# Kernel tuning notes

Hardware: AMD Instinct MI355X
Metric: run time of the kernel (lower is better)

## Reference

```python
import jax, jax.numpy as jnp
import numpy as np

BLOCK = 64       # _aether_cfg['block_size']
JL_DIM = 32      # epsilon_jl_bridge d_out
EPS_GOV = 0.5    # fixed governor eps (governor.target)
ROPE_BASE = 10000.0
RMS_EPS = 1e-6


def _normalize(x, axis=-1):
    n = jnp.sqrt(jnp.sum(x * x, axis=axis, keepdims=True))
    return x / jnp.maximum(n, 1e-12)


def _rms_norm(x):
    return x * jax.lax.rsqrt(jnp.mean(x * x, axis=-1, keepdims=True) + RMS_EPS)


def _rope(x, cos, sin):
    half = x.shape[-1] // 2
    x1, x2 = x[..., :half], x[..., half:]
    return jnp.concatenate([x1 * cos + x2 * sin, -x1 * sin + x2 * cos], axis=-1)


def setup_inputs() -> dict:
    key = jax.random.key(0)
    ks = jax.random.split(key, 6)
    B, S, Dm, H = 2, 2048, 2048, 16
    sc = 1.0 / np.sqrt(Dm)
    x = jax.random.normal(ks[0], (B, S, Dm), jnp.float32)
    Wq = jax.random.normal(ks[1], (Dm, Dm), jnp.float32) * sc
    Wk = jax.random.normal(ks[2], (Dm, Dm), jnp.float32) * sc
    Wv = jax.random.normal(ks[3], (Dm, Dm), jnp.float32) * sc
    Wo = jax.random.normal(ks[4], (Dm, Dm), jnp.float32) * sc
    q_gain = jnp.ones((H,), jnp.float32)
    return {"x": x, "Wq": Wq, "Wk": Wk, "Wv": Wv, "Wo": Wo, "q_gain": q_gain}


def reference(x, Wq, Wk, Wv, Wo, q_gain):
    B, S, Dm = x.shape
    H = q_gain.shape[0]
    Dh = Dm // H

    # QKV projections (bias-free linear, torch weight layout [out,in])
    q = (x @ Wq.T).reshape(B, S, H, Dh).transpose(0, 2, 1, 3)  # (B,H,S,Dh)
    k = (x @ Wk.T).reshape(B, S, H, Dh).transpose(0, 2, 1, 3)
    v = (x @ Wv.T).reshape(B, S, H, Dh).transpose(0, 2, 1, 3)

    # RoPE tables
    inv_freq = 1.0 / (ROPE_BASE ** (jnp.arange(0, Dh, 2, dtype=jnp.float32) / Dh))
    freqs = jnp.outer(jnp.arange(S, dtype=jnp.float32), inv_freq)  # (S,Dh/2)
    cos = jnp.cos(freqs)[None, None]
    sin = jnp.sin(freqs)[None, None]

    q = _rope(_rms_norm(q), cos, sin) * q_gain[None, :, None, None]
    k = _rope(_rms_norm(k), cos, sin)

    # --- aether sparse SDPA: JL block bounds -> top-k blocks -> gather -> SDPA ---
    N = S // BLOCK  # number of KV blocks (static)
    proj = jax.random.normal(jax.random.key(42), (Dh, JL_DIM), jnp.float32) / np.sqrt(JL_DIM)

    q_proj = _normalize(q.mean(axis=2, keepdims=True) @ proj)          # (B,H,1,JL)
    k_blocks = k.reshape(B, H, N, BLOCK, Dh)
    k_proj = _normalize(k_blocks @ proj)                               # (B,H,N,BLOCK,JL)
    centroids = _normalize(k_proj.mean(axis=3))                        # (B,H,N,JL)
    radii = jnp.clip(
        1.0 - jnp.min(jnp.sum(k_proj * centroids[:, :, :, None, :], axis=-1), axis=-1),
        0.0, 1.0)                                                      # (B,H,N)
    ub = jnp.einsum('bhqj,bhnj->bhqn', q_proj, centroids) + radii[:, :, None, :]
    scores = ub[:, :, 0, :]                                            # (B,H,N)
    # force-include the last two blocks (union in the original code)
    scores = scores.at[:, :, N - 2:].set(jnp.inf)

    n_keep = max(2, int(N * min(1.0, EPS_GOV))) + 2                    # static
    _, top_idx = jax.lax.top_k(scores, n_keep)                         # (B,H,n_keep)
    top_idx = jnp.sort(top_idx, axis=-1)
    idx = (top_idx[..., None] * BLOCK + jnp.arange(BLOCK)).reshape(B, H, -1)  # (B,H,K)

    k_s = jnp.take_along_axis(k, idx[..., None], axis=2)               # (B,H,K,Dh)
    v_s = jnp.take_along_axis(v, idx[..., None], axis=2)

    att = jax.nn.softmax(
        jnp.einsum('bhqd,bhkd->bhqk', q, k_s) / np.sqrt(Dh), axis=-1)  # (B,H,S,K)
    y = jnp.einsum('bhqk,bhkd->bhqd', att, v_s)                        # (B,H,S,Dh)

    y = y.transpose(0, 2, 1, 3).reshape(B, S, Dm)
    return y @ Wo.T
```

## Files before the change

kernel.cpp:

```cpp
#include <hip/hip_runtime.h>
#include <hip/hip_bf16.h>

#define B_ 2
#define S_ 2048
#define DM 2048
#define H_ 16
#define DH 128
#define NBLK 32
#define NKEEP 18
#define BH (B_ * H_)

typedef __attribute__((ext_vector_type(8))) short short8;
typedef __attribute__((ext_vector_type(8))) _Float16 f16x8;
typedef __attribute__((ext_vector_type(4))) _Float16 f16x4;
typedef __attribute__((ext_vector_type(4))) float f32x4;

#define GLOAD16(gp, lp)                                                        \
  __builtin_amdgcn_global_load_lds(                                            \
      (const __attribute__((address_space(1))) unsigned int*)(const void*)(gp),\
      (__attribute__((address_space(3))) unsigned int*)(void*)(lp), 16, 0, 0)

__device__ __forceinline__ unsigned short f32_to_bf16(float f) {
  unsigned u = __float_as_uint(f);
  unsigned r = (u + 0x7fffu + ((u >> 16) & 1u)) >> 16;
  return (unsigned short)r;
}
__device__ __forceinline__ float bf16_to_f32(unsigned short h) {
  return __uint_as_float(((unsigned)h) << 16);
}

__device__ __forceinline__ unsigned rotl32(unsigned x, int r) {
  return (x << r) | (x >> (32 - r));
}

__device__ __forceinline__ float erfinv_f32(float x) {
  float w = -log1pf(-x * x);
  float p;
  if (w < 5.0f) {
    w -= 2.5f;
    p = 2.81022636e-08f;
    p = fmaf(p, w, 3.43273939e-07f);
    p = fmaf(p, w, -3.5233877e-06f);
    p = fmaf(p, w, -4.39150654e-06f);
    p = fmaf(p, w, 0.00021858087f);
    p = fmaf(p, w, -0.00125372503f);
    p = fmaf(p, w, -0.00417768164f);
    p = fmaf(p, w, 0.246640727f);
    p = fmaf(p, w, 1.50140941f);
  } else {
    w = sqrtf(w) - 3.0f;
    p = -0.000200214257f;
    p = fmaf(p, w, 0.000100950558f);
    p = fmaf(p, w, 0.00134934322f);
    p = fmaf(p, w, -0.00367342844f);
    p = fmaf(p, w, 0.00573950773f);
    p = fmaf(p, w, -0.0076224613f);
    p = fmaf(p, w, 0.00943887047f);
    p = fmaf(p, w, 1.00167406f);
    p = fmaf(p, w, 2.83297682f);
  }
  return p * x;
}

__device__ __forceinline__ float bits_to_normal(unsigned b) {
  float f = __uint_as_float((b >> 9) | 0x3f800000u) - 1.0f;
  const float lo = -0.9999999403953552f;
  float u = fmaxf(lo, fmaf(f, 2.0f, lo));
  return 1.4142135623730951f * erfinv_f32(u);
}

__global__ void proj_kernel(float* __restrict__ proj) {
  int i = blockIdx.x * blockDim.x + threadIdx.x;
  if (i >= 4096) return;
  unsigned k0 = 0u, k1 = 42u;
  unsigned k2 = 0x1BD11BDAu ^ k0 ^ k1;
  unsigned x0 = 0u, x1 = (unsigned)i;
  x0 += k0; x1 += k1;
#define QR(r) { x0 += x1; x1 = rotl32(x1, r); x1 ^= x0; }
  QR(13) QR(15) QR(26) QR(6)   x0 += k1; x1 += k2 + 1u;
  QR(17) QR(29) QR(16) QR(24)  x0 += k2; x1 += k0 + 2u;
  QR(13) QR(15) QR(26) QR(6)   x0 += k0; x1 += k1 + 3u;
  QR(17) QR(29) QR(16) QR(24)  x0 += k1; x1 += k2 + 4u;
  QR(13) QR(15) QR(26) QR(6)   x0 += k2; x1 += k0 + 5u;
#undef QR
  proj[i] = bits_to_normal(x0 ^ x1) / 5.656854249492381f;
}

__global__ void rope_table_kernel(float* __restrict__ cosb, float* __restrict__ sinb) {
  int s = blockIdx.x;
  int j = threadIdx.x;
  double e = (double)(2 * j) / 128.0;
  double invf = 1.0 / pow(10000.0, e);
  float freq = (float)s * (float)invf;
  cosb[s * 64 + j] = (float)cos((double)freq);
  sinb[s * 64 + j] = (float)sin((double)freq);
}

__global__ __launch_bounds__(256) void split_x3_kernel(const float* __restrict__ in,
                                                       unsigned short* __restrict__ hi,
                                                       unsigned short* __restrict__ lo,
                                                       _Float16* __restrict__ f16,
                                                       int n4) {
  int i = blockIdx.x * blockDim.x + threadIdx.x;
  if (i >= n4) return;
  float4 v = ((const float4*)in)[i];
  ushort4 hv, lv;
  f16x4 fv;
  hv.x = f32_to_bf16(v.x); lv.x = f32_to_bf16(v.x - bf16_to_f32(hv.x)); fv[0] = (_Float16)v.x;
  hv.y = f32_to_bf16(v.y); lv.y = f32_to_bf16(v.y - bf16_to_f32(hv.y)); fv[1] = (_Float16)v.y;
  hv.z = f32_to_bf16(v.z); lv.z = f32_to_bf16(v.z - bf16_to_f32(hv.z)); fv[2] = (_Float16)v.z;
  hv.w = f32_to_bf16(v.w); lv.w = f32_to_bf16(v.w - bf16_to_f32(hv.w)); fv[3] = (_Float16)v.w;
  ((ushort4*)hi)[i] = hv;
  ((ushort4*)lo)[i] = lv;
  ((f16x4*)f16)[i] = fv;
}

__global__ __launch_bounds__(256) void split_kernel(const float* __restrict__ in,
                                                    unsigned short* __restrict__ hi,
                                                    unsigned short* __restrict__ lo,
                                                    int n4) {
  int i = blockIdx.x * blockDim.x + threadIdx.x;
  if (i >= n4) return;
  float4 v = ((const float4*)in)[i];
  ushort4 hv, lv;
  hv.x = f32_to_bf16(v.x); lv.x = f32_to_bf16(v.x - bf16_to_f32(hv.x));
  hv.y = f32_to_bf16(v.y); lv.y = f32_to_bf16(v.y - bf16_to_f32(hv.y));
  hv.z = f32_to_bf16(v.z); lv.z = f32_to_bf16(v.z - bf16_to_f32(hv.z));
  hv.w = f32_to_bf16(v.w); lv.w = f32_to_bf16(v.w - bf16_to_f32(hv.w));
  ((ushort4*)hi)[i] = hv;
  ((ushort4*)lo)[i] = lv;
}

__global__ __launch_bounds__(256) void split_f16_kernel(const float* __restrict__ in,
                                                        _Float16* __restrict__ f16,
                                                        int n4) {
  int i = blockIdx.x * blockDim.x + threadIdx.x;
  if (i >= n4) return;
  float4 v = ((const float4*)in)[i];
  f16x4 fv;
  fv[0] = (_Float16)v.x; fv[1] = (_Float16)v.y;
  fv[2] = (_Float16)v.z; fv[3] = (_Float16)v.w;
  ((f16x4*)f16)[i] = fv;
}

__global__ __launch_bounds__(512, 2) void mfma_gemm_k_sk(const unsigned short* __restrict__ Ahi,
                                                         const unsigned short* __restrict__ Alo,
                                                         const unsigned short* __restrict__ Whi,
                                                         const unsigned short* __restrict__ Wlo,
                                                         float* __restrict__ kp0,
                                                         float* __restrict__ kp1) {
  __shared__ char smem[131072];
  const int t = threadIdx.x, l = t & 63, w = t >> 6;
  const int lin = blockIdx.z * 128 + blockIdx.y * 8 + blockIdx.x;
  const int swz = (lin & 7) * 32 + (lin >> 3);
  const int kz = swz >> 7;
  const int idx = swz & 127;
  const int n0 = (idx & 7) * 256;
  const int m0 = (idx >> 3) * 256;
  const int kbase = kz * 1024;
  float* C = kz ? kp1 : kp0;
  const int wm = w >> 2, wn = w & 3;
  const int lr = l & 15;
  const int lg8 = (l >> 4) * 8;
  const size_t rstep = (size_t)16 * DM;

  const unsigned short* gAh = Ahi + (size_t)(m0 + w * 32 + lr) * DM + lg8;
  const unsigned short* gAl = Alo + (size_t)(m0 + w * 32 + lr) * DM + lg8;
  const unsigned short* gBh = Whi + (size_t)(n0 + w * 32 + lr) * DM + lg8;
  const unsigned short* gBl = Wlo + (size_t)(n0 + w * 32 + lr) * DM + lg8;

  auto STAGE = [&](int k0, int c) {
    char* base = smem + c * 65536 + w * 2048;
    GLOAD16(gAh + k0, base);
    GLOAD16(gAh + rstep + k0, base + 1024);
    GLOAD16(gAl + k0, base + 16384);
    GLOAD16(gAl + rstep + k0, base + 16384 + 1024);
    GLOAD16(gBh + k0, base + 32768);
    GLOAD16(gBh + rstep + k0, base + 32768 + 1024);
    GLOAD16(gBl + k0, base + 49152);
    GLOAD16(gBl + rstep + k0, base + 49152 + 1024);
  };

  f32x4 acc[8][4];
#pragma unroll
  for (int i = 0; i < 8; ++i)
#pragma unroll
    for (int j = 0; j < 4; ++j) acc[i][j] = (f32x4){0.f, 0.f, 0.f, 0.f};

  STAGE(kbase, 0);
  int cur = 0;

  for (int k0 = kbase; k0 < kbase + 1024; k0 += 32) {
    if (k0 + 32 < kbase + 1024) {
      STAGE(k0 + 32, cur ^ 1);
      asm volatile("s_waitcnt vmcnt(8)" ::: "memory");
    } else {
      asm volatile("s_waitcnt vmcnt(0)" ::: "memory");
    }
    __builtin_amdgcn_s_barrier();

    char* buf = smem + cur * 65536;
    short8 bh[4], bl[4];
#pragma unroll
    for (int f = 0; f < 4; ++f) {
      bh[f] = *(const short8*)(buf + 32768 + (wn * 4 + f) * 1024 + l * 16);
      bl[f] = *(const short8*)(buf + 49152 + (wn * 4 + f) * 1024 + l * 16);
    }
    __builtin_amdgcn_s_setprio(1);
#pragma unroll
    for (int mp = 0; mp < 4; ++mp) {
      short8 ah0 = *(const short8*)(buf + (wm * 8 + 2 * mp) * 1024 + l * 16);
      short8 ah1 = *(const short8*)(buf + (wm * 8 + 2 * mp + 1) * 1024 + l * 16);
      short8 al0 = *(const short8*)(buf + 16384 + (wm * 8 + 2 * mp) * 1024 + l * 16);
      short8 al1 = *(const short8*)(buf + 16384 + (wm * 8 + 2 * mp + 1) * 1024 + l * 16);
#pragma unroll
      for (int n = 0; n < 4; ++n) {
        acc[2 * mp][n] = __builtin_amdgcn_mfma_f32_16x16x32_bf16(ah0, bh[n], acc[2 * mp][n], 0, 0, 0);
        acc[2 * mp][n] = __builtin_amdgcn_mfma_f32_16x16x32_bf16(ah0, bl[n], acc[2 * mp][n], 0, 0, 0);
        acc[2 * mp][n] = __builtin_amdgcn_mfma_f32_16x16x32_bf16(al0, bh[n], acc[2 * mp][n], 0, 0, 0);
      }
#pragma unroll
      for (int n = 0; n < 4; ++n) {
        acc[2 * mp + 1][n] = __builtin_amdgcn_mfma_f32_16x16x32_bf16(ah1, bh[n], acc[2 * mp + 1][n], 0, 0, 0);
        acc[2 * mp + 1][n] = __builtin_amdgcn_mfma_f32_16x16x32_bf16(ah1, bl[n], acc[2 * mp + 1][n], 0, 0, 0);
        acc[2 * mp + 1][n] = __builtin_amdgcn_mfma_f32_16x16x32_bf16(al1, bh[n], acc[2 * mp + 1][n], 0, 0, 0);
      }
    }
    __builtin_amdgcn_s_setprio(0);
    __builtin_amdgcn_s_barrier();
    cur ^= 1;
  }

#pragma unroll
  for (int m = 0; m < 8; ++m) {
    int row0 = m0 + wm * 128 + m * 16 + (l >> 4) * 4;
#pragma unroll
    for (int n = 0; n < 4; ++n) {
      int col = n0 + wn * 64 + n * 16 + (l & 15);
      int h = col >> 7, d = col & 127;
#pragma unroll
      for (int r = 0; r < 4; ++r) {
        int mm = row0 + r;
        int b = mm >> 11, s = mm & (S_ - 1);
        C[(((size_t)(b * H_ + h) * S_) + s) * DH + d] = acc[m][n][r];
      }
    }
  }
}

__global__ __launch_bounds__(512, 2) void mfma_gemm_qv(const _Float16* __restrict__ A,
                                                       const _Float16* __restrict__ W,
                                                       float* __restrict__ Cq,
                                                       _Float16* __restrict__ vt) {
  __shared__ char smem[65536];
  const int t = threadIdx.x, l = t & 63, w = t >> 6;
  const int lin = blockIdx.y * gridDim.x + blockIdx.x;
  const int swz = (lin & 7) * 32 + (lin >> 3);
  const int n0 = (swz & 15) * 256;
  const int m0 = (swz >> 4) * 256;
  const int wm = w >> 2, wn = w & 3;
  const int lr = l & 15;
  const int lg8 = (l >> 4) * 8;
  const size_t rstep = (size_t)16 * DM;

  const _Float16* gA = A + (size_t)(m0 + w * 32 + lr) * DM + lg8;
  const _Float16* gB = W + (size_t)(n0 + w * 32 + lr) * DM + lg8;

  auto STAGE = [&](int k0, int c) {
    char* base = smem + c * 32768 + w * 2048;
    GLOAD16(gA + k0, base);
    GLOAD16(gA + rstep + k0, base + 1024);
    GLOAD16(gB + k0, base + 16384);
    GLOAD16(gB + rstep + k0, base + 16384 + 1024);
  };

  f32x4 acc[8][4];
#pragma unroll
  for (int i = 0; i < 8; ++i)
#pragma unroll
    for (int j = 0; j < 4; ++j) acc[i][j] = (f32x4){0.f, 0.f, 0.f, 0.f};

  STAGE(0, 0);
  int cur = 0;

  for (int k0 = 0; k0 < DM; k0 += 32) {
    if (k0 + 32 < DM) {
      STAGE(k0 + 32, cur ^ 1);
      asm volatile("s_waitcnt vmcnt(4)" ::: "memory");
    } else {
      asm volatile("s_waitcnt vmcnt(0)" ::: "memory");
    }
    __builtin_amdgcn_s_barrier();

    char* buf = smem + cur * 32768;
    f16x8 b[4];
#pragma unroll
    for (int j = 0; j < 4; ++j)
      b[j] = *(const f16x8*)(buf + 16384 + (wn * 4 + j) * 1024 + l * 16);
    __builtin_amdgcn_s_setprio(1);
#pragma unroll
    for (int i = 0; i < 8; ++i) {
      f16x8 a = *(const f16x8*)(buf + (wm * 8 + i) * 1024 + l * 16);
#pragma unroll
      for (int j = 0; j < 4; ++j)
        acc[i][j] = __builtin_amdgcn_mfma_f32_16x16x32_f16(a, b[j], acc[i][j], 0, 0, 0);
    }
    __builtin_amdgcn_s_setprio(0);
    __builtin_amdgcn_s_barrier();
    cur ^= 1;
  }

#pragma unroll
  for (int m = 0; m < 8; ++m) {
    int row0 = m0 + wm * 128 + m * 16 + (l >> 4) * 4;
#pragma unroll
    for (int n = 0; n < 4; ++n) {
      int col = n0 + wn * 64 + n * 16 + (l & 15);
      if (col < DM) {
        int h = col >> 7, d = col & 127;
#pragma unroll
        for (int r = 0; r < 4; ++r) {
          int mm = row0 + r;
          int b2 = mm >> 11, s = mm & (S_ - 1);
          Cq[(((size_t)(b2 * H_ + h) * S_) + s) * DH + d] = acc[m][n][r];
        }
      } else {
        int vcol = col - DM;
        int h = vcol >> 7, d = vcol & 127;
        int b2 = row0 >> 11, s0 = row0 & (S_ - 1);
        f16x4 vv;
        vv[0] = (_Float16)acc[m][n][0];
        vv[1] = (_Float16)acc[m][n][1];
        vv[2] = (_Float16)acc[m][n][2];
        vv[3] = (_Float16)acc[m][n][3];
        *(f16x4*)(vt + (((size_t)(b2 * H_ + h)) * DH + d) * S_ + s0) = vv;
      }
    }
  }
}

template <int MODE>
__global__ __launch_bounds__(256) void mfma_gemm_f16(const _Float16* __restrict__ A,
                                                     const _Float16* __restrict__ W,
                                                     void* __restrict__ Cout) {
  __shared__ char smem[65536];
  const int t = threadIdx.x, l = t & 63, w = t >> 6;
  const int lin = blockIdx.y * gridDim.x + blockIdx.x;
  const int cpx = (gridDim.x * gridDim.y) >> 3;
  const int swz = (lin & 7) * cpx + (lin >> 3);
  const int n0 = (swz % gridDim.x) * 128;
  const int m0 = (swz / gridDim.x) * 128;
  const int wm = w >> 1, wn = w & 1;
  const int lr = l & 15;
  const int lg8 = (l >> 4) * 8;

  auto STAGE = [&](int k0, int c) {
    char* base = smem + c * 32768;
#pragma unroll
    for (int f0 = 0; f0 < 4; ++f0) {
      int f = w * 4 + f0;
      int rb = f >> 1, kh = f & 1;
      GLOAD16(A + (size_t)(m0 + rb * 16 + lr) * DM + k0 + kh * 32 + lg8,
              base + f * 1024);
      GLOAD16(W + (size_t)(n0 + rb * 16 + lr) * DM + k0 + kh * 32 + lg8,
              base + 16384 + f * 1024);
    }
  };

  f32x4 acc[4][4];
#pragma unroll
  for (int i = 0; i < 4; ++i)
#pragma unroll
    for (int j = 0; j < 4; ++j) acc[i][j] = (f32x4){0.f, 0.f, 0.f, 0.f};

  STAGE(0, 0);
  int cur = 0;

  for (int k0 = 0; k0 < DM; k0 += 64) {
    if (k0 + 64 < DM) {
      STAGE(k0 + 64, cur ^ 1);
      asm volatile("s_waitcnt vmcnt(8)" ::: "memory");
    } else {
      asm volatile("s_waitcnt vmcnt(0)" ::: "memory");
    }
    __builtin_amdgcn_s_barrier();

    char* buf = smem + cur * 32768;
    f16x8 a[4][2], b[4][2];
#pragma unroll
    for (int i = 0; i < 4; ++i)
#pragma unroll
      for (int kh = 0; kh < 2; ++kh) {
        a[i][kh] = *(const f16x8*)(buf + ((wm * 4 + i) * 2 + kh) * 1024 + l * 16);
        b[i][kh] = *(const f16x8*)(buf + 16384 + ((wn * 4 + i) * 2 + kh) * 1024 + l * 16);
      }
    __builtin_amdgcn_s_setprio(1);
#pragma unroll
    for (int i = 0; i < 4; ++i)
#pragma unroll
      for (int j = 0; j < 4; ++j) {
        acc[i][j] = __builtin_amdgcn_mfma_f32_16x16x32_f16(a[i][0], b[j][0], acc[i][j], 0, 0, 0);
        acc[i][j] = __builtin_amdgcn_mfma_f32_16x16x32_f16(a[i][1], b[j][1], acc[i][j], 0, 0, 0);
      }
    __builtin_amdgcn_s_setprio(0);
    __builtin_amdgcn_s_barrier();
    cur ^= 1;
  }

#pragma unroll
  for (int i = 0; i < 4; ++i) {
    int row0 = m0 + wm * 64 + i * 16 + (l >> 4) * 4;
#pragma unroll
    for (int j = 0; j < 4; ++j) {
      int col = n0 + wn * 64 + j * 16 + (l & 15);
      if constexpr (MODE == 1) {
        float* C = (float*)Cout;
#pragma unroll
        for (int r = 0; r < 4; ++r)
          C[(size_t)(row0 + r) * DM + col] = acc[i][j][r];
      }
    }
  }
}

__global__ __launch_bounds__(256) void rmsrope_k_kernel(float* __restrict__ k,
                                                        const float* __restrict__ kp1,
                                                        _Float16* __restrict__ kf,
                                                        const float* __restrict__ cosb,
                                                        const float* __restrict__ sinb) {
  int w = threadIdx.x >> 6;
  int lane = threadIdx.x & 63;
  long r = (long)blockIdx.x * 4 + w;
  float* p = k + r * DH;
  const float* p1 = kp1 + r * DH;
  int s = (int)(r & (S_ - 1));
  float x1 = p[lane] + p1[lane];
  float x2 = p[lane + 64] + p1[lane + 64];
  float ss = fmaf(x1, x1, x2 * x2);
#pragma unroll
  for (int off = 32; off; off >>= 1) ss += __shfl_xor(ss, off);
  float rms = rsqrtf(ss * (1.0f / 128.0f) + 1e-6f);
  float n1 = x1 * rms, n2 = x2 * rms;
  float c = cosb[s * 64 + lane], sn = sinb[s * 64 + lane];
  float o1 = fmaf(n1, c, n2 * sn);
  float o2 = fmaf(-n1, sn, n2 * c);
  p[lane] = o1;
  p[lane + 64] = o2;
  kf[r * DH + lane] = (_Float16)o1;
  kf[r * DH + lane + 64] = (_Float16)o2;
}

__global__ __launch_bounds__(256) void rmsrope_q_kernel(float* __restrict__ q,
                                                        const float* __restrict__ cosb,
                                                        const float* __restrict__ sinb,
                                                        const float* __restrict__ qg) {
  int w = threadIdx.x >> 6;
  int lane = threadIdx.x & 63;
  long r = (long)blockIdx.x * 4 + w;
  float* p = q + r * DH;
  int s = (int)(r & (S_ - 1));
  int h = (int)((r >> 11) & (H_ - 1));
  float x1 = p[lane], x2 = p[lane + 64];
  float ss = fmaf(x1, x1, x2 * x2);
#pragma unroll
  for (int off = 32; off; off >>= 1) ss += __shfl_xor(ss, off);
  float rms = rsqrtf(ss * (1.0f / 128.0f) + 1e-6f);
  float n1 = x1 * rms, n2 = x2 * rms;
  float c = cosb[s * 64 + lane], sn = sinb[s * 64 + lane];
  float g = qg[h];
  float o1 = fmaf(n1, c, n2 * sn) * g;
  float o2 = fmaf(-n1, sn, n2 * c) * g;
  p[lane] = o1;
  p[lane + 64] = o2;
}

__global__ __launch_bounds__(256) void qmean_part_kernel(const float* __restrict__ q,
                                                         float* __restrict__ partial) {
  __shared__ float red[256];
  const int bh = blockIdx.x >> 4, chunk = blockIdx.x & 15;
  const int t = threadIdx.x;
  const int d = t & 127, half = t >> 7;
  const float* qb = q + ((size_t)bh * S_ + chunk * 128 + half * 64) * DH;
  float sum = 0.0f;
#pragma unroll 4
  for (int s = 0; s < 64; ++s) sum += qb[(size_t)s * DH + d];
  red[t] = sum;
  __syncthreads();
  if (t < 128) partial[(size_t)blockIdx.x * 128 + t] = red[t] + red[t + 128];
}

__global__ void qproj_kernel(const float* __restrict__ partial,
                             const float* __restrict__ proj,
                             float* __restrict__ qp) {
  __shared__ float meanq[128];
  __shared__ float qps[32];
  __shared__ float nrm;
  const int bh = blockIdx.x, t = threadIdx.x;
  float s = 0.0f;
#pragma unroll
  for (int c = 0; c < 16; ++c) s += partial[((size_t)bh * 16 + c) * 128 + t];
  meanq[t] = s * (1.0f / 2048.0f);
  __syncthreads();
  if (t < 32) {
    float sum = 0.0f;
    for (int d = 0; d < 128; ++d) sum = fmaf(meanq[d], proj[d * 32 + t], sum);
    qps[t] = sum;
  }
  __syncthreads();
  if (t == 0) {
    float sum = 0.0f;
    for (int j = 0; j < 32; ++j) sum += qps[j] * qps[j];
    nrm = 1.0f / fmaxf(sqrtf(sum), 1e-12f);
  }
  __syncthreads();
  if (t < 32) qp[bh * 32 + t] = qps[t] * nrm;
}

__global__ __launch_bounds__(256) void kscore_kernel(const float* __restrict__ k,
                                                     const float* __restrict__ proj,
                                                     const float* __restrict__ qp,
                                                     float* __restrict__ scores) {
  __shared__ float ps[128][32];
  __shared__ float kp[64][33];
  __shared__ float cent[33];
  __shared__ float nrm;
  const int bh = blockIdx.x >> 5, n = blockIdx.x & 31;
  const int t = threadIdx.x;
  for (int i = t; i < 4096; i += 256) ps[i >> 5][i & 31] = proj[i];
  const float* kn = k + ((size_t)bh * S_ + n * 64) * DH;
  __syncthreads();
  {
    int row = t >> 2, j0 = (t & 3) * 8;
    float accv[8];
#pragma unroll
    for (int jj = 0; jj < 8; ++jj) accv[jj] = 0.0f;
#pragma unroll 4
    for (int d = 0; d < 128; ++d) {
      float kv = kn[(size_t)row * DH + d];
#pragma unroll
      for (int jj = 0; jj < 8; ++jj) accv[jj] = fmaf(kv, ps[d][j0 + jj], accv[jj]);
    }
#pragma unroll
    for (int jj = 0; jj < 8; ++jj) kp[row][j0 + jj] = accv[jj];
  }
  __syncthreads();
  if (t < 64) {
    float sum = 0.0f;
    for (int j = 0; j < 32; ++j) sum += kp[t][j] * kp[t][j];
    float scl = 1.0f / fmaxf(sqrtf(sum), 1e-12f);
    for (int j = 0; j < 32; ++j) kp[t][j] *= scl;
  }
  __syncthreads();
  if (t < 32) {
    float sum = 0.0f;
    for (int r2 = 0; r2 < 64; ++r2) sum += kp[r2][t];
    cent[t] = sum * (1.0f / 64.0f);
  }
  __syncthreads();
  if (t == 0) {
    float sum = 0.0f;
    for (int j = 0; j < 32; ++j) sum += cent[j] * cent[j];
    nrm = 1.0f / fmaxf(sqrtf(sum), 1e-12f);
  }
  __syncthreads();
  if (t < 32) cent[t] *= nrm;
  __syncthreads();
  if (t < 64) {
    float dt = 0.0f;
    for (int j = 0; j < 32; ++j) dt = fmaf(kp[t][j], cent[j], dt);
#pragma unroll
    for (int off = 32; off; off >>= 1) dt = fminf(dt, __shfl_xor(dt, off));
    if (t == 0) {
      float radius = fminf(fmaxf(1.0f - dt, 0.0f), 1.0f);
      float dq = 0.0f;
      for (int j = 0; j < 32; ++j) dq = fmaf(qp[bh * 32 + j], cent[j], dq);
      scores[bh * 32 + n] = dq + radius;
    }
  }
}

__global__ void topk_kernel(const float* __restrict__ scores, int* __restrict__ top_idx) {
  if (threadIdx.x != 0) return;
  const int bh = blockIdx.x;
  float sc[NBLK];
  for (int j = 0; j < NBLK; ++j) sc[j] = scores[bh * 32 + j];
  sc[NBLK - 2] = INFINITY;
  sc[NBLK - 1] = INFINITY;
  int chosen[NKEEP];
  bool used[NBLK];
  for (int j = 0; j < NBLK; ++j) used[j] = false;
  for (int kk = 0; kk < NKEEP; ++kk) {
    int best = -1;
    float bv = 0.0f;
    for (int j = 0; j < NBLK; ++j)
      if (!used[j] && (best < 0 || sc[j] > bv)) { bv = sc[j]; best = j; }
    used[best] = true;
    chosen[kk] = best;
  }
  for (int a = 1; a < NKEEP; ++a) {
    int v2 = chosen[a], b2 = a - 1;
    while (b2 >= 0 && chosen[b2] > v2) { chosen[b2 + 1] = chosen[b2]; --b2; }
    chosen[b2 + 1] = v2;
  }
  for (int a = 0; a < NKEEP; ++a) top_idx[bh * NKEEP + a] = chosen[a];
}

__global__ __launch_bounds__(256) void attn_mfma_kernel(const float* __restrict__ q,
                                                        const _Float16* __restrict__ kf,
                                                        const _Float16* __restrict__ vt,
                                                        const int* __restrict__ top_idx,
                                                        _Float16* __restrict__ yf) {
  __shared__ char lds[74752];
  const int bh = blockIdx.x >> 5;
  const int qt = blockIdx.x & 31;
  const int t = threadIdx.x, l = t & 63, w = t >> 6;
  const int lr = l & 15, lg = l >> 4;
  const float scale = 0.08838834764831843f;

  f16x8 qf[4];
  {
    const float* qbase = q + ((size_t)(bh * S_ + qt * 64 + w * 16 + lr)) * DH + lg * 8;
#pragma unroll
    for (int dc = 0; dc < 4; ++dc) {
      float4 v0 = *(const float4*)(qbase + dc * 32);
      float4 v1 = *(const float4*)(qbase + dc * 32 + 4);
      f16x8 h;
      h[0] = (_Float16)v0.x; h[1] = (_Float16)v0.y; h[2] = (_Float16)v0.z; h[3] = (_Float16)v0.w;
      h[4] = (_Float16)v1.x; h[5] = (_Float16)v1.y; h[6] = (_Float16)v1.z; h[7] = (_Float16)v1.w;
      qf[dc] = h;
    }
  }

  float m_[4] = {-INFINITY, -INFINITY, -INFINITY, -INFINITY};
  float ls[4] = {0.f, 0.f, 0.f, 0.f};
  f32x4 yacc[8];
#pragma unroll
  for (int dt = 0; dt < 8; ++dt) yacc[dt] = (f32x4){0.f, 0.f, 0.f, 0.f};

  char* Pw = lds + 65536 + w * 2304;

  const _Float16* kb0 = kf + (size_t)bh * S_ * DH;
  const _Float16* vb0 = vt + (size_t)bh * DH * S_;
  const int* idxp = top_idx + bh * NKEEP;

  auto STAGE = [&](int blk, int c) {
    char* base = lds + c * 32768;
#pragma unroll
    for (int f0 = 0; f0 < 4; ++f0) {
      int f = w * 4 + f0;
      int kt = f >> 2, dc = f & 3;
      GLOAD16(kb0 + (size_t)(blk * 64 + kt * 16 + lr) * DH + dc * 32 + lg * 8,
              base + f * 1024);
      int K0 = f >> 3, dt = f & 7;
      GLOAD16(vb0 + (size_t)(dt * 16 + lr) * S_ + blk * 64 + K0 * 32 + lg * 8,
              base + 16384 + f * 1024);
    }
  };

  int cur = 0;
  STAGE(idxp[0], 0);

  for (int it = 0; it < NKEEP; ++it) {
    if (it + 1 < NKEEP) {
      STAGE(idxp[it + 1], cur ^ 1);
      asm volatile("s_waitcnt vmcnt(8)" ::: "memory");
    } else {
      asm volatile("s_waitcnt vmcnt(0)" ::: "memory");
    }
    __builtin_amdgcn_s_barrier();
    char* buf = lds + cur * 32768;

    f32x4 sacc[4];
#pragma unroll
    for (int kt = 0; kt < 4; ++kt) sacc[kt] = (f32x4){0.f, 0.f, 0.f, 0.f};
    __builtin_amdgcn_s_setprio(1);
#pragma unroll
    for (int kt = 0; kt < 4; ++kt)
#pragma unroll
      for (int dc = 0; dc < 4; ++dc) {
        f16x8 kfr = *(const f16x8*)(buf + (kt * 4 + dc) * 1024 + l * 16);
        sacc[kt] = __builtin_amdgcn_mfma_f32_16x16x32_f16(qf[dc], kfr, sacc[kt], 0, 0, 0);
      }
    __builtin_amdgcn_s_setprio(0);

    float p[4][4];
#pragma unroll
    for (int r = 0; r < 4; ++r) {
      float mt = fmaxf(fmaxf(sacc[0][r], sacc[1][r]), fmaxf(sacc[2][r], sacc[3][r])) * scale;
#pragma unroll
      for (int off = 1; off < 16; off <<= 1) mt = fmaxf(mt, __shfl_xor(mt, off));
      float mn = fmaxf(m_[r], mt);
      float corr = __expf(m_[r] - mn);
      float rs = 0.f;
#pragma unroll
      for (int kt = 0; kt < 4; ++kt) {
        p[kt][r] = __expf(fmaf(sacc[kt][r], scale, -mn));
        rs += p[kt][r];
      }
#pragma unroll
      for (int off = 1; off < 16; off <<= 1) rs += __shfl_xor(rs, off);
      ls[r] = ls[r] * corr + rs;
      m_[r] = mn;
#pragma unroll
      for (int dt = 0; dt < 8; ++dt) yacc[dt][r] *= corr;
    }

#pragma unroll
    for (int kt = 0; kt < 4; ++kt)
#pragma unroll
      for (int r = 0; r < 4; ++r)
        *(_Float16*)(Pw + (lg * 4 + r) * 144 + (kt * 16 + lr) * 2) = (_Float16)p[kt][r];

    __builtin_amdgcn_s_setprio(1);
#pragma unroll
    for (int K0 = 0; K0 < 2; ++K0) {
      f16x8 pa = *(const f16x8*)(Pw + lr * 144 + K0 * 64 + lg * 16);
#pragma unroll
      for (int dt = 0; dt < 8; ++dt) {
        f16x8 vf = *(const f16x8*)(buf + 16384 + (K0 * 8 + dt) * 1024 + l * 16);
        yacc[dt] = __builtin_amdgcn_mfma_f32_16x16x32_f16(pa, vf, yacc[dt], 0, 0, 0);
      }
    }
    __builtin_amdgcn_s_setprio(0);

    __builtin_amdgcn_s_barrier();
    cur ^= 1;
  }

  const int b = bh >> 4, h = bh & (H_ - 1);
  float inv[4];
#pragma unroll
  for (int r = 0; r < 4; ++r) inv[r] = 1.0f / ls[r];
#pragma unroll
  for (int r = 0; r < 4; ++r) {
    int srow = qt * 64 + w * 16 + lg * 4 + r;
    size_t off0 = ((size_t)b * S_ + srow) * DM + h * DH + lr;
#pragma unroll
    for (int dt = 0; dt < 8; ++dt)
      yf[off0 + dt * 16] = (_Float16)(yacc[dt][r] * inv[r]);
  }
}

extern "C" void kernel_launch(void* const* d_in, const int* in_sizes, int n_in,
                              void* d_out, int out_size, void* d_ws, size_t ws_size,
                              hipStream_t stream) {
  const float* x  = (const float*)d_in[0];
  const float* Wq = (const float*)d_in[1];
  const float* Wk = (const float*)d_in[2];
  const float* Wv = (const float*)d_in[3];
  const float* Wo = (const float*)d_in[4];
  const float* qg = (const float*)d_in[5];
  float* out = (float*)d_out;

  const size_t NE = (size_t)BH * S_ * DH;
  const size_t WE = (size_t)DM * DM;
  char* p = (char*)d_ws;
  float* q_ws = (float*)p; p += NE * 4;
  float* k_ws = (float*)p; p += NE * 4;
  unsigned short* xhi = (unsigned short*)p; p += NE * 2;
  unsigned short* xlo = (unsigned short*)p; p += NE * 2;
  _Float16* xf16 = (_Float16*)p; p += NE * 2;
  unsigned short* wkhi = (unsigned short*)p; p += WE * 2;
  unsigned short* wklo = (unsigned short*)p; p += WE * 2;
  _Float16* wqv = (_Float16*)p; p += 2 * WE * 2;
  float* cosb = (float*)p; p += (size_t)S_ * 64 * 4;
  float* sinb = (float*)p; p += (size_t)S_ * 64 * 4;
  float* projb = (float*)p; p += 4096 * 4;
  int* idxb = (int*)p; p += BH * NKEEP * 4;
  float* scores = (float*)p; p += BH * NBLK * 4;
  float* qpbuf = (float*)p; p += BH * 32 * 4;
  float* qpart = cosb;
  float* kpart1 = q_ws;
  _Float16* kf16 = (_Float16*)wkhi;
  _Float16* vt = (_Float16*)xlo;
  _Float16* yf16 = (_Float16*)xhi;
  _Float16* wo = wqv;

  const int nx4 = (int)(NE / 4);
  const int nw4 = (int)(WE / 4);

  proj_kernel<<<dim3(16), dim3(256), 0, stream>>>(projb);
  rope_table_kernel<<<dim3(S_), dim3(64), 0, stream>>>(cosb, sinb);
  split_x3_kernel<<<dim3(nx4 / 256), dim3(256), 0, stream>>>(x, xhi, xlo, xf16, nx4);
  split_kernel<<<dim3(nw4 / 256), dim3(256), 0, stream>>>(Wk, wkhi, wklo, nw4);
  split_f16_kernel<<<dim3(nw4 / 256), dim3(256), 0, stream>>>(Wq, wqv, nw4);
  split_f16_kernel<<<dim3(nw4 / 256), dim3(256), 0, stream>>>(Wv, wqv + WE, nw4);

  mfma_gemm_k_sk<<<dim3(8, 16, 2), dim3(512), 0, stream>>>(xhi, xlo, wkhi, wklo,
                                                           k_ws, kpart1);

  rmsrope_k_kernel<<<dim3((BH * S_) / 4), dim3(256), 0, stream>>>(k_ws, kpart1, kf16, cosb, sinb);

  mfma_gemm_qv<<<dim3(16, 16), dim3(512), 0, stream>>>(xf16, wqv, q_ws, vt);

  rmsrope_q_kernel<<<dim3((BH * S_) / 4), dim3(256), 0, stream>>>(q_ws, cosb, sinb, qg);

  qmean_part_kernel<<<dim3(BH * 16), dim3(256), 0, stream>>>(q_ws, qpart);
  qproj_kernel<<<dim3(BH), dim3(128), 0, stream>>>(qpart, projb, qpbuf);
  kscore_kernel<<<dim3(BH * NBLK), dim3(256), 0, stream>>>(k_ws, projb, qpbuf, scores);
  topk_kernel<<<dim3(BH), dim3(64), 0, stream>>>(scores, idxb);

  attn_mfma_kernel<<<dim3(BH * 32), dim3(256), 0, stream>>>(q_ws, kf16, vt, idxb, yf16);

  split_f16_kernel<<<dim3(nw4 / 256), dim3(256), 0, stream>>>(Wo, wo, nw4);
  mfma_gemm_f16<1><<<dim3(16, 32), dim3(256), 0, stream>>>(yf16, wo, out);
}
```

Before: 463.3 us.

## Interleave next-tile global-to-LDS loads with MFMA phases in GEMM main loops

Splits the per-iteration prefetch of the next K tile into pieces issued between sub-phases of the MFMA compute, in both the split-bf16 K-projection GEMM and the f16 Q/V GEMM. Each phase is separated by barriers. The goal is to spread global memory traffic across the compute instead of issuing it all at once before the loop body. In exchange it adds more barriers per iteration, and it relies on the waitcnt counts staying correct for the loads already in flight.

```diff
diff --git a/kernel.cpp b/kernel.cpp
--- a/kernel.cpp
+++ b/kernel.cpp
@@ -169,67 +169,95 @@
   const unsigned short* gBh = Whi + (size_t)(n0 + w * 32 + lr) * DM + lg8;
   const unsigned short* gBl = Wlo + (size_t)(n0 + w * 32 + lr) * DM + lg8;
 
-  auto STAGE = [&](int k0, int c) {
-    char* base = smem + c * 65536 + w * 2048;
-    GLOAD16(gAh + k0, base);
-    GLOAD16(gAh + rstep + k0, base + 1024);
-    GLOAD16(gAl + k0, base + 16384);
-    GLOAD16(gAl + rstep + k0, base + 16384 + 1024);
-    GLOAD16(gBh + k0, base + 32768);
-    GLOAD16(gBh + rstep + k0, base + 32768 + 1024);
-    GLOAD16(gBl + k0, base + 49152);
-    GLOAD16(gBl + rstep + k0, base + 49152 + 1024);
-  };
-
   f32x4 acc[8][4];
 #pragma unroll
   for (int i = 0; i < 8; ++i)
 #pragma unroll
     for (int j = 0; j < 4; ++j) acc[i][j] = (f32x4){0.f, 0.f, 0.f, 0.f};
 
-  STAGE(kbase, 0);
+  {
+    char* base = smem + w * 2048;
+    GLOAD16(gAh + kbase, base);
+    GLOAD16(gAh + rstep + kbase, base + 1024);
+    GLOAD16(gAl + kbase, base + 16384);
+    GLOAD16(gAl + rstep + kbase, base + 16384 + 1024);
+    GLOAD16(gBh + kbase, base + 32768);
+    GLOAD16(gBh + rstep + kbase, base + 32768 + 1024);
+    GLOAD16(gBl + kbase, base + 49152);
+    GLOAD16(gBl + rstep + kbase, base + 49152 + 1024);
+  }
   int cur = 0;
 
+#define KQUAD(q)                                                                        \
+  {                                                                                     \
+    short8 ah0 = *(const short8*)(buf + (wm * 8 + 2 * (q)) * 1024 + l * 16);            \
+    short8 ah1 = *(const short8*)(buf + (wm * 8 + 2 * (q) + 1) * 1024 + l * 16);        \
+    short8 al0 = *(const short8*)(buf + 16384 + (wm * 8 + 2 * (q)) * 1024 + l * 16);    \
+    short8 al1 = *(const short8*)(buf + 16384 + (wm * 8 + 2 * (q) + 1) * 1024 + l * 16);\
+    __builtin_amdgcn_s_setprio(1);                                                      \
+    _Pragma("unroll")                                                                   \
+    for (int n = 0; n < 4; ++n) {                                                       \
+      acc[2 * (q)][n] = __builtin_amdgcn_mfma_f32_16x16x32_bf16(ah0, bh[n], acc[2 * (q)][n], 0, 0, 0); \
+      acc[2 * (q)][n] = __builtin_amdgcn_mfma_f32_16x16x32_bf16(ah0, bl[n], acc[2 * (q)][n], 0, 0, 0); \
+      acc[2 * (q)][n] = __builtin_amdgcn_mfma_f32_16x16x32_bf16(al0, bh[n], acc[2 * (q)][n], 0, 0, 0); \
+    }                                                                                   \
+    _Pragma("unroll")                                                                   \
+    for (int n = 0; n < 4; ++n) {                                                       \
+      acc[2 * (q) + 1][n] = __builtin_amdgcn_mfma_f32_16x16x32_bf16(ah1, bh[n], acc[2 * (q) + 1][n], 0, 0, 0); \
+      acc[2 * (q) + 1][n] = __builtin_amdgcn_mfma_f32_16x16x32_bf16(ah1, bl[n], acc[2 * (q) + 1][n], 0, 0, 0); \
+      acc[2 * (q) + 1][n] = __builtin_amdgcn_mfma_f32_16x16x32_bf16(al1, bh[n], acc[2 * (q) + 1][n], 0, 0, 0); \
+    }                                                                                   \
+    __builtin_amdgcn_s_setprio(0);                                                      \
+  }
+
   for (int k0 = kbase; k0 < kbase + 1024; k0 += 32) {
-    if (k0 + 32 < kbase + 1024) {
-      STAGE(k0 + 32, cur ^ 1);
-      asm volatile("s_waitcnt vmcnt(8)" ::: "memory");
+    const bool more = (k0 + 32 < kbase + 1024);
+    char* buf = smem + cur * 65536;
+    char* nb = smem + (cur ^ 1) * 65536 + w * 2048;
+    const int kn = k0 + 32;
+
+    if (more) {
+      GLOAD16(gBh + kn, nb + 32768);
+      GLOAD16(gBh + rstep + kn, nb + 32768 + 1024);
+      asm volatile("s_waitcnt vmcnt(2)" ::: "memory");
     } else {
       asm volatile("s_waitcnt vmcnt(0)" ::: "memory");
     }
     __builtin_amdgcn_s_barrier();
 
-    char* buf = smem + cur * 65536;
     short8 bh[4], bl[4];
 #pragma unroll
     for (int f = 0; f < 4; ++f) {
       bh[f] = *(const short8*)(buf + 32768 + (wn * 4 + f) * 1024 + l * 16);
       bl[f] = *(const short8*)(buf + 49152 + (wn * 4 + f) * 1024 + l * 16);
     }
-    __builtin_amdgcn_s_setprio(1);
-#pragma unroll
-    for (int mp = 0; mp < 4; ++mp) {
-      short8 ah0 = *(const short8*)(buf + (wm * 8 + 2 * mp) * 1024 + l * 16);
-      short8 ah1 = *(const short8*)(buf + (wm * 8 + 2 * mp + 1) * 1024 + l * 16);
-      short8 al0 = *(const short8*)(buf + 16384 + (wm * 8 + 2 * mp) * 1024 + l * 16);
-      short8 al1 = *(const short8*)(buf + 16384 + (wm * 8 + 2 * mp + 1) * 1024 + l * 16);
-#pragma unroll
-      for (int n = 0; n < 4; ++n) {
-        acc[2 * mp][n] = __builtin_amdgcn_mfma_f32_16x16x32_bf16(ah0, bh[n], acc[2 * mp][n], 0, 0, 0);
-        acc[2 * mp][n] = __builtin_amdgcn_mfma_f32_16x16x32_bf16(ah0, bl[n], acc[2 * mp][n], 0, 0, 0);
-        acc[2 * mp][n] = __builtin_amdgcn_mfma_f32_16x16x32_bf16(al0, bh[n], acc[2 * mp][n], 0, 0, 0);
-      }
-#pragma unroll
-      for (int n = 0; n < 4; ++n) {
-        acc[2 * mp + 1][n] = __builtin_amdgcn_mfma_f32_16x16x32_bf16(ah1, bh[n], acc[2 * mp + 1][n], 0, 0, 0);
-        acc[2 * mp + 1][n] = __builtin_amdgcn_mfma_f32_16x16x32_bf16(ah1, bl[n], acc[2 * mp + 1][n], 0, 0, 0);
-        acc[2 * mp + 1][n] = __builtin_amdgcn_mfma_f32_16x16x32_bf16(al1, bh[n], acc[2 * mp + 1][n], 0, 0, 0);
-      }
-    }
-    __builtin_amdgcn_s_setprio(0);
-    __builtin_amdgcn_s_barrier();
+    KQUAD(0);
+    __builtin_amdgcn_s_barrier();
+
+    if (more) {
+      GLOAD16(gBl + kn, nb + 49152);
+      GLOAD16(gBl + rstep + kn, nb + 49152 + 1024);
+    }
+    KQUAD(1);
+    __builtin_amdgcn_s_barrier();
+
+    if (more) {
+      GLOAD16(gAh + kn, nb);
+      GLOAD16(gAh + rstep + kn, nb + 1024);
+    }
+    KQUAD(2);
+    __builtin_amdgcn_s_barrier();
+
+    if (more) {
+      GLOAD16(gAl + kn, nb + 16384);
+      GLOAD16(gAl + rstep + kn, nb + 16384 + 1024);
+    }
+    KQUAD(3);
+    __builtin_amdgcn_s_barrier();
+
     cur ^= 1;
   }
+#undef KQUAD
 
 #pragma unroll
   for (int m = 0; m < 8; ++m) {
@@ -266,40 +294,43 @@
   const _Float16* gA = A + (size_t)(m0 + w * 32 + lr) * DM + lg8;
   const _Float16* gB = W + (size_t)(n0 + w * 32 + lr) * DM + lg8;
 
-  auto STAGE = [&](int k0, int c) {
-    char* base = smem + c * 32768 + w * 2048;
-    GLOAD16(gA + k0, base);
-    GLOAD16(gA + rstep + k0, base + 1024);
-    GLOAD16(gB + k0, base + 16384);
-    GLOAD16(gB + rstep + k0, base + 16384 + 1024);
-  };
-
   f32x4 acc[8][4];
 #pragma unroll
   for (int i = 0; i < 8; ++i)
 #pragma unroll
     for (int j = 0; j < 4; ++j) acc[i][j] = (f32x4){0.f, 0.f, 0.f, 0.f};
 
-  STAGE(0, 0);
+  {
+    char* base = smem + w * 2048;
+    GLOAD16(gA, base);
+    GLOAD16(gA + rstep, base + 1024);
+    GLOAD16(gB, base + 16384);
+    GLOAD16(gB + rstep, base + 16384 + 1024);
+  }
   int cur = 0;
 
   for (int k0 = 0; k0 < DM; k0 += 32) {
-    if (k0 + 32 < DM) {
-      STAGE(k0 + 32, cur ^ 1);
-      asm volatile("s_waitcnt vmcnt(4)" ::: "memory");
+    const bool more = (k0 + 32 < DM);
+    char* buf = smem + cur * 32768;
+    char* nb = smem + (cur ^ 1) * 32768 + w * 2048;
+    const int kn = k0 + 32;
+
+    if (more) {
+      GLOAD16(gA + kn, nb);
+      GLOAD16(gA + rstep + kn, nb + 1024);
+      asm volatile("s_waitcnt vmcnt(2)" ::: "memory");
     } else {
       asm volatile("s_waitcnt vmcnt(0)" ::: "memory");
     }
     __builtin_amdgcn_s_barrier();
 
-    char* buf = smem + cur * 32768;
     f16x8 b[4];
 #pragma unroll
     for (int j = 0; j < 4; ++j)
       b[j] = *(const f16x8*)(buf + 16384 + (wn * 4 + j) * 1024 + l * 16);
     __builtin_amdgcn_s_setprio(1);
 #pragma unroll
-    for (int i = 0; i < 8; ++i) {
+    for (int i = 0; i < 4; ++i) {
       f16x8 a = *(const f16x8*)(buf + (wm * 8 + i) * 1024 + l * 16);
 #pragma unroll
       for (int j = 0; j < 4; ++j)
@@ -307,6 +338,22 @@
     }
     __builtin_amdgcn_s_setprio(0);
     __builtin_amdgcn_s_barrier();
+
+    if (more) {
+      GLOAD16(gB + kn, nb + 16384);
+      GLOAD16(gB + rstep + kn, nb + 16384 + 1024);
+    }
+    __builtin_amdgcn_s_setprio(1);
+#pragma unroll
+    for (int i = 4; i < 8; ++i) {
+      f16x8 a = *(const f16x8*)(buf + (wm * 8 + i) * 1024 + l * 16);
+#pragma unroll
+      for (int j = 0; j < 4; ++j)
+        acc[i][j] = __builtin_amdgcn_mfma_f32_16x16x32_f16(a, b[j], acc[i][j], 0, 0, 0);
+    }
+    __builtin_amdgcn_s_setprio(0);
+    __builtin_amdgcn_s_barrier();
+
     cur ^= 1;
   }
 
```

Result: faster. 448.5 us (-3.2%).
